# Optimization experiments

Measured on AMD Instinct MI355X. Metric: run time of the kernel, lower is better.

Reference implementation:

```python
import jax, jax.numpy as jnp
import numpy as np

V, D, H, O = 500000, 64, 64, 64
N0, N1, N2, K = 8192, 100000, 300000, 32


def setup_inputs() -> dict:
    key = jax.random.key(0)
    ks = jax.random.split(key, 8)
    return {
        "feats": jax.random.normal(ks[0], (V, D), dtype=jnp.float32),
        "W0": jax.random.normal(ks[1], (D, H), dtype=jnp.float32) / jnp.sqrt(jnp.float32(D)),
        "b0": jnp.zeros((H,), jnp.float32),
        "W1": jax.random.normal(ks[2], (H, O), dtype=jnp.float32) / jnp.sqrt(jnp.float32(H)),
        "b1": jnp.zeros((O,), jnp.float32),
        "neigh_idx0": jax.random.randint(ks[3], (N0, K), 0, N1),  # seed -> positions in 1-hop layer
        "neigh_idx1": jax.random.randint(ks[4], (N1, K), 0, N2),  # 1-hop -> positions in 2-hop layer
        "node_ids1": jax.random.randint(ks[5], (N1,), 0, V),      # 1-hop node ids into feature table
        "node_ids2": jax.random.randint(ks[6], (N2,), 0, V),      # 2-hop node ids into feature table
    }


def reference(feats, W0, b0, W1, b1, neigh_idx0, neigh_idx1, node_ids1, node_ids2):
    # Embedding lookups (self.features(...)) for hop-1 and hop-2 node layers.
    v1 = feats[node_ids1]                       # [N1, D]
    v2 = feats[node_ids2]                       # [N2, D]
    # Layer i=0, hop=1: mean over sampled neighbors (mask.mm == gather-mean),
    # then linear0 + relu (dropout in eval mode == identity).
    agg1 = jnp.mean(v2[neigh_idx1], axis=1)     # [N1, D]
    h1 = jax.nn.relu(agg1 @ W0 + b0)            # [N1, H]
    # Layer i=1, hop=0: aggregate hop-1 representations for seed nodes, linear1 + relu.
    agg0 = jnp.mean(h1[neigh_idx0], axis=1)     # [N0, H]
    out = jax.nn.relu(agg0 @ W1 + b1)           # [N0, O]
    return out
```

## Files before the change

### kernel.cpp

```cpp
#include <hip/hip_runtime.h>
#include <hip/hip_bf16.h>

typedef __hip_bfloat16 bf16;

static __device__ __forceinline__ float lane_bcast_f(float v, int l) {
    return __uint_as_float(__builtin_amdgcn_readlane(__float_as_uint(v), l));
}

static __device__ __forceinline__ float4 load4f(const float* p) {
    return *(const float4*)p;
}
static __device__ __forceinline__ float4 load4f(const bf16* p) {
    const ushort4 s = *(const ushort4*)p;
    float4 r;
    r.x = __uint_as_float((unsigned)s.x << 16);
    r.y = __uint_as_float((unsigned)s.y << 16);
    r.z = __uint_as_float((unsigned)s.z << 16);
    r.w = __uint_as_float((unsigned)s.w << 16);
    return r;
}

template <typename HT>
__global__ __launch_bounds__(256) void k_hop1(
    const float* __restrict__ feats,
    const float* __restrict__ W0,
    const float* __restrict__ b0,
    const int*   __restrict__ idx1,
    const int*   __restrict__ nid2,
    HT*          __restrict__ h1,
    int N1)
{
    const int lane = threadIdx.x & 63;
    const int sub  = lane >> 4;
    const int c4   = lane & 15;
    const int gwave = blockIdx.x * (blockDim.x >> 6) + (threadIdx.x >> 6);
    const int nwave = gridDim.x * (blockDim.x >> 6);

    float w0c[64];
#pragma unroll
    for (int d = 0; d < 64; ++d) w0c[d] = W0[d * 64 + lane];
    const float bias = b0[lane];

    const float4* f4 = (const float4*)feats;

    for (int base = 2 * gwave; base < N1; base += 2 * nwave) {
        const int r0 = base;
        const bool has_r1 = (base + 1 < N1);
        const int r1 = has_r1 ? base + 1 : base;

        int nk0[8], nk1[8];
#pragma unroll
        for (int i = 0; i < 8; ++i) {
            nk0[i] = idx1[r0 * 32 + 4 * i + sub];
            nk1[i] = idx1[r1 * 32 + 4 * i + sub];
        }
#pragma unroll
        for (int i = 0; i < 8; ++i) {
            nk0[i] = nid2[nk0[i]];
            nk1[i] = nid2[nk1[i]];
        }

        float a0[4] = {0.f, 0.f, 0.f, 0.f};
        float a1[4] = {0.f, 0.f, 0.f, 0.f};
#pragma unroll
        for (int i = 0; i < 8; ++i) {
            const float4 v0 = f4[(size_t)nk0[i] * 16 + c4];
            const float4 v1 = f4[(size_t)nk1[i] * 16 + c4];
            a0[0] += v0.x; a0[1] += v0.y; a0[2] += v0.z; a0[3] += v0.w;
            a1[0] += v1.x; a1[1] += v1.y; a1[2] += v1.z; a1[3] += v1.w;
        }

#pragma unroll
        for (int c = 0; c < 4; ++c) {
            a0[c] += __shfl_xor(a0[c], 16, 64);
            a0[c] += __shfl_xor(a0[c], 32, 64);
            a1[c] += __shfl_xor(a1[c], 16, 64);
            a1[c] += __shfl_xor(a1[c], 32, 64);
            a0[c] *= 0.03125f;
            a1[c] *= 0.03125f;
        }

        float h0 = bias, h1v = bias;
#pragma unroll
        for (int d = 0; d < 64; ++d) {
            h0  = fmaf(lane_bcast_f(a0[d & 3], d >> 2), w0c[d], h0);
            h1v = fmaf(lane_bcast_f(a1[d & 3], d >> 2), w0c[d], h1v);
        }
        h0  = fmaxf(h0, 0.f);
        h1v = fmaxf(h1v, 0.f);

        if constexpr (sizeof(HT) == 2) {
            h1[(size_t)r0 * 64 + lane] = __float2bfloat16(h0);
            if (has_r1) h1[(size_t)r1 * 64 + lane] = __float2bfloat16(h1v);
        } else {
            h1[(size_t)r0 * 64 + lane] = h0;
            if (has_r1) h1[(size_t)r1 * 64 + lane] = h1v;
        }
    }
}

template <typename HT>
__global__ __launch_bounds__(256) void k_hop0(
    const HT*    __restrict__ h1,
    const float* __restrict__ W1,
    const float* __restrict__ b1,
    const int*   __restrict__ idx0,
    float*       __restrict__ out,
    int N0)
{
    const int lane = threadIdx.x & 63;
    const int sub  = lane >> 4;
    const int c4   = lane & 15;
    const int gwave = blockIdx.x * (blockDim.x >> 6) + (threadIdx.x >> 6);
    const int nwave = gridDim.x * (blockDim.x >> 6);

    float w1c[64];
#pragma unroll
    for (int d = 0; d < 64; ++d) w1c[d] = W1[d * 64 + lane];
    const float bias = b1[lane];

    for (int row = gwave; row < N0; row += nwave) {
        int jk[8];
#pragma unroll
        for (int i = 0; i < 8; ++i) jk[i] = idx0[row * 32 + 4 * i + sub];

        float a[4] = {0.f, 0.f, 0.f, 0.f};
#pragma unroll
        for (int i = 0; i < 8; ++i) {
            const float4 v = load4f(h1 + (size_t)jk[i] * 64 + c4 * 4);
            a[0] += v.x; a[1] += v.y; a[2] += v.z; a[3] += v.w;
        }
#pragma unroll
        for (int c = 0; c < 4; ++c) {
            a[c] += __shfl_xor(a[c], 16, 64);
            a[c] += __shfl_xor(a[c], 32, 64);
            a[c] *= 0.03125f;
        }

        float o = bias;
#pragma unroll
        for (int d = 0; d < 64; ++d)
            o = fmaf(lane_bcast_f(a[d & 3], d >> 2), w1c[d], o);
        out[(size_t)row * 64 + lane] = fmaxf(o, 0.f);
    }
}

extern "C" void kernel_launch(void* const* d_in, const int* in_sizes, int n_in,
                              void* d_out, int out_size, void* d_ws, size_t ws_size,
                              hipStream_t stream) {
    const float* feats = (const float*)d_in[0];
    const float* W0    = (const float*)d_in[1];
    const float* b0    = (const float*)d_in[2];
    const float* W1    = (const float*)d_in[3];
    const float* b1    = (const float*)d_in[4];
    const int*   idx0  = (const int*)d_in[5];
    const int*   idx1  = (const int*)d_in[6];
    const int*   nid2  = (const int*)d_in[8];

    const int N0 = in_sizes[5] / 32;
    const int N1 = in_sizes[6] / 32;

    const size_t need_f32 = (size_t)N1 * 64 * sizeof(float);

    if (ws_size >= need_f32) {
        float* h1 = (float*)d_ws;
        k_hop1<float><<<2048, 256, 0, stream>>>(feats, W0, b0, idx1, nid2, h1, N1);
        k_hop0<float><<<2048, 256, 0, stream>>>(h1, W1, b1, idx0, (float*)d_out, N0);
    } else {
        bf16* h1 = (bf16*)d_ws;
        k_hop1<bf16><<<2048, 256, 0, stream>>>(feats, W0, b0, idx1, nid2, h1, N1);
        k_hop0<bf16><<<2048, 256, 0, stream>>>(h1, W1, b1, idx0, (float*)d_out, N0);
    }
}
```

Before: 316.6 us.

## Pre-gather hop-2 features into a bf16 table and store h1 as bf16

```diff
diff --git a/kernel.cpp b/kernel.cpp
--- a/kernel.cpp
+++ b/kernel.cpp
@@ -7,11 +7,16 @@
     return __uint_as_float(__builtin_amdgcn_readlane(__float_as_uint(v), l));
 }
 
-static __device__ __forceinline__ float4 load4f(const float* p) {
-    return *(const float4*)p;
-}
-static __device__ __forceinline__ float4 load4f(const bf16* p) {
-    const ushort4 s = *(const ushort4*)p;
+static __device__ __forceinline__ unsigned short f2bf_bits(float x) {
+    bf16 h = __float2bfloat16(x);
+    return *(unsigned short*)&h;
+}
+
+static __device__ __forceinline__ float4 tload4(const float* p, size_t row, int c4) {
+    return ((const float4*)p)[row * 16 + c4];
+}
+static __device__ __forceinline__ float4 tload4(const unsigned short* p, size_t row, int c4) {
+    const ushort4 s = ((const ushort4*)p)[row * 16 + c4];
     float4 r;
     r.x = __uint_as_float((unsigned)s.x << 16);
     r.y = __uint_as_float((unsigned)s.y << 16);
@@ -20,14 +25,44 @@
     return r;
 }
 
-template <typename HT>
+__global__ __launch_bounds__(256) void k_cast(
+    const float* __restrict__ feats,
+    const int*   __restrict__ nid2,
+    unsigned short* __restrict__ feats2,
+    int N2)
+{
+    const int lane = threadIdx.x & 63;
+    const int sub  = lane >> 4;
+    const int c4   = lane & 15;
+    const int gwave = blockIdx.x * (blockDim.x >> 6) + (threadIdx.x >> 6);
+    const int nwave = gridDim.x * (blockDim.x >> 6);
+
+    for (int base = 8 * gwave; base < N2; base += 8 * nwave) {
+        const int t0 = base + sub;
+        const int t1 = base + 4 + sub;
+        const bool v0 = (t0 < N2), v1 = (t1 < N2);
+        const int n0 = v0 ? nid2[t0] : 0;
+        const int n1 = v1 ? nid2[t1] : 0;
+        const float4 a = tload4(feats, (size_t)n0, c4);
+        const float4 b = tload4(feats, (size_t)n1, c4);
+        ushort4 sa, sb;
+        sa.x = f2bf_bits(a.x); sa.y = f2bf_bits(a.y);
+        sa.z = f2bf_bits(a.z); sa.w = f2bf_bits(a.w);
+        sb.x = f2bf_bits(b.x); sb.y = f2bf_bits(b.y);
+        sb.z = f2bf_bits(b.z); sb.w = f2bf_bits(b.w);
+        if (v0) ((ushort4*)feats2)[(size_t)t0 * 16 + c4] = sa;
+        if (v1) ((ushort4*)feats2)[(size_t)t1 * 16 + c4] = sb;
+    }
+}
+
+template <bool IND, typename TT>
 __global__ __launch_bounds__(256) void k_hop1(
-    const float* __restrict__ feats,
+    const TT*    __restrict__ table,
     const float* __restrict__ W0,
     const float* __restrict__ b0,
     const int*   __restrict__ idx1,
     const int*   __restrict__ nid2,
-    HT*          __restrict__ h1,
+    unsigned short* __restrict__ h1,
     int N1)
 {
     const int lane = threadIdx.x & 63;
@@ -41,8 +76,6 @@
     for (int d = 0; d < 64; ++d) w0c[d] = W0[d * 64 + lane];
     const float bias = b0[lane];
 
-    const float4* f4 = (const float4*)feats;
-
     for (int base = 2 * gwave; base < N1; base += 2 * nwave) {
         const int r0 = base;
         const bool has_r1 = (base + 1 < N1);
@@ -54,18 +87,20 @@
             nk0[i] = idx1[r0 * 32 + 4 * i + sub];
             nk1[i] = idx1[r1 * 32 + 4 * i + sub];
         }
-#pragma unroll
-        for (int i = 0; i < 8; ++i) {
-            nk0[i] = nid2[nk0[i]];
-            nk1[i] = nid2[nk1[i]];
+        if constexpr (IND) {
+#pragma unroll
+            for (int i = 0; i < 8; ++i) {
+                nk0[i] = nid2[nk0[i]];
+                nk1[i] = nid2[nk1[i]];
+            }
         }
 
         float a0[4] = {0.f, 0.f, 0.f, 0.f};
         float a1[4] = {0.f, 0.f, 0.f, 0.f};
 #pragma unroll
         for (int i = 0; i < 8; ++i) {
-            const float4 v0 = f4[(size_t)nk0[i] * 16 + c4];
-            const float4 v1 = f4[(size_t)nk1[i] * 16 + c4];
+            const float4 v0 = tload4(table, (size_t)nk0[i], c4);
+            const float4 v1 = tload4(table, (size_t)nk1[i], c4);
             a0[0] += v0.x; a0[1] += v0.y; a0[2] += v0.z; a0[3] += v0.w;
             a1[0] += v1.x; a1[1] += v1.y; a1[2] += v1.z; a1[3] += v1.w;
         }
@@ -89,19 +124,13 @@
         h0  = fmaxf(h0, 0.f);
         h1v = fmaxf(h1v, 0.f);
 
-        if constexpr (sizeof(HT) == 2) {
-            h1[(size_t)r0 * 64 + lane] = __float2bfloat16(h0);
-            if (has_r1) h1[(size_t)r1 * 64 + lane] = __float2bfloat16(h1v);
-        } else {
-            h1[(size_t)r0 * 64 + lane] = h0;
-            if (has_r1) h1[(size_t)r1 * 64 + lane] = h1v;
-        }
-    }
-}
-
-template <typename HT>
+        h1[(size_t)r0 * 64 + lane] = f2bf_bits(h0);
+        if (has_r1) h1[(size_t)r1 * 64 + lane] = f2bf_bits(h1v);
+    }
+}
+
 __global__ __launch_bounds__(256) void k_hop0(
-    const HT*    __restrict__ h1,
+    const unsigned short* __restrict__ h1,
     const float* __restrict__ W1,
     const float* __restrict__ b1,
     const int*   __restrict__ idx0,
@@ -127,7 +156,7 @@
         float a[4] = {0.f, 0.f, 0.f, 0.f};
 #pragma unroll
         for (int i = 0; i < 8; ++i) {
-            const float4 v = load4f(h1 + (size_t)jk[i] * 64 + c4 * 4);
+            const float4 v = tload4(h1, (size_t)jk[i], c4);
             a[0] += v.x; a[1] += v.y; a[2] += v.z; a[3] += v.w;
         }
 #pragma unroll
@@ -159,16 +188,22 @@
 
     const int N0 = in_sizes[5] / 32;
     const int N1 = in_sizes[6] / 32;
-
-    const size_t need_f32 = (size_t)N1 * 64 * sizeof(float);
-
-    if (ws_size >= need_f32) {
-        float* h1 = (float*)d_ws;
-        k_hop1<float><<<2048, 256, 0, stream>>>(feats, W0, b0, idx1, nid2, h1, N1);
-        k_hop0<float><<<2048, 256, 0, stream>>>(h1, W1, b1, idx0, (float*)d_out, N0);
+    const int N2 = in_sizes[8];
+
+    const size_t bytes_feats2 = (size_t)N2 * 64 * 2;
+    const size_t bytes_h1     = (size_t)N1 * 64 * 2;
+
+    if (ws_size >= bytes_feats2 + bytes_h1) {
+        unsigned short* feats2 = (unsigned short*)d_ws;
+        unsigned short* h1     = (unsigned short*)((char*)d_ws + bytes_feats2);
+        k_cast<<<2048, 256, 0, stream>>>(feats, nid2, feats2, N2);
+        k_hop1<false, unsigned short><<<2048, 256, 0, stream>>>(
+            feats2, W0, b0, idx1, nullptr, h1, N1);
+        k_hop0<<<2048, 256, 0, stream>>>(h1, W1, b1, idx0, (float*)d_out, N0);
     } else {
-        bf16* h1 = (bf16*)d_ws;
-        k_hop1<bf16><<<2048, 256, 0, stream>>>(feats, W0, b0, idx1, nid2, h1, N1);
-        k_hop0<bf16><<<2048, 256, 0, stream>>>(h1, W1, b1, idx0, (float*)d_out, N0);
-    }
-}
+        unsigned short* h1 = (unsigned short*)d_ws;
+        k_hop1<true, float><<<2048, 256, 0, stream>>>(
+            feats, W0, b0, idx1, nid2, h1, N1);
+        k_hop0<<<2048, 256, 0, stream>>>(h1, W1, b1, idx0, (float*)d_out, N0);
+    }
+}
```

Result: faster. 270.9 us (-14.4%).
